# Performance work log

Measured on AMD Instinct MI355X. Metric: run time of the kernel, lower is better.

## Reference

```python
import jax, jax.numpy as jnp
import numpy as np

EMBED_DIM = 1024
HEAD_DIM = 64
B, S = 8, 2048


def setup_inputs() -> dict:
    key = jax.random.key(0)
    ks = jax.random.split(key, 8)
    s_in = 1.0 / np.sqrt(EMBED_DIM)
    return {
        "x": jax.random.normal(ks[0], (B, S, EMBED_DIM), dtype=jnp.float32),
        "y": jax.random.normal(ks[1], (B, S, EMBED_DIM), dtype=jnp.float32),
        "Wq": jax.random.normal(ks[2], (EMBED_DIM, HEAD_DIM), dtype=jnp.float32) * s_in,
        "bq": jnp.zeros((HEAD_DIM,), dtype=jnp.float32),
        "Wk": jax.random.normal(ks[3], (EMBED_DIM, HEAD_DIM), dtype=jnp.float32) * s_in,
        "bk": jnp.zeros((HEAD_DIM,), dtype=jnp.float32),
        "Wv": jax.random.normal(ks[4], (EMBED_DIM, HEAD_DIM), dtype=jnp.float32) * s_in,
        "bv": jnp.zeros((HEAD_DIM,), dtype=jnp.float32),
    }


def reference(x, y, Wq, bq, Wk, bk, Wv, bv):
    # single-head attention; mask=True -> tril applied PRE-softmax (zeros, not -inf)
    q = jnp.einsum("bse,eh->bsh", y, Wq) + bq  # [B,S,H]
    k = jnp.einsum("bse,eh->bsh", x, Wk) + bk
    v = jnp.einsum("bse,eh->bsh", x, Wv) + bv
    scale = 1.0 / jnp.sqrt(jnp.float32(HEAD_DIM))
    scores = jnp.einsum("bqh,bkh->bqk", q, k) * scale  # [B,S,S]
    scores = jnp.tril(scores)  # faithful: zero upper triangle BEFORE softmax
    attn = jax.nn.softmax(scores, axis=-1)
    return jnp.einsum("bqk,bkh->bqh", attn, v)  # [B,S,H]
```

## Files before the change

### kernel.cpp

```cpp
#include <hip/hip_runtime.h>

#define SEQ 2048
#define EMB 1024
#define HD 64

typedef _Float16 f16x8 __attribute__((ext_vector_type(8)));
typedef _Float16 f16x4 __attribute__((ext_vector_type(4)));
typedef float f32x4 __attribute__((ext_vector_type(4)));

__device__ __forceinline__ f32x4 mfma32(f16x8 a, f16x8 b, f32x4 c) {
    return __builtin_amdgcn_mfma_f32_16x16x32_f16(a, b, c, 0, 0, 0);
}
__device__ __forceinline__ f32x4 mfma16(f16x4 a, f16x4 b, f32x4 c) {
    return __builtin_amdgcn_mfma_f32_16x16x16f16(a, b, c, 0, 0, 0);
}

__global__ __launch_bounds__(256) void wcvt_kernel(
    const float* __restrict__ Wq, const float* __restrict__ Wk,
    const float* __restrict__ Wv, _Float16* __restrict__ Wf)
{
    const int m = blockIdx.x >> 2, nt = blockIdx.x & 3;
    const float* __restrict__ W = (m == 0) ? Wq : (m == 1) ? Wk : Wv;
    const int tid = threadIdx.x;
    #pragma unroll
    for (int i = 0; i < 8; ++i) {
        int linear = i * 256 + tid;
        int kc = linear >> 6, ln = linear & 63;
        int q8 = (ln >> 4) * 8, l = ln & 15;
        f16x8 w;
        #pragma unroll
        for (int j = 0; j < 8; ++j)
            w[j] = (_Float16)W[(size_t)(kc * 32 + q8 + j) * 64 + nt * 16 + l];
        *(f16x8*)&Wf[((size_t)((m * 4 + nt) * 32 + kc)) * 512 + (size_t)ln * 8] = w;
    }
}

__global__ __launch_bounds__(512) void proj_kernel(
    const float* __restrict__ x, const float* __restrict__ y,
    const _Float16* __restrict__ Wf,
    const float* __restrict__ bq, const float* __restrict__ bk,
    const float* __restrict__ bv,
    _Float16* __restrict__ Qb, _Float16* __restrict__ Kf,
    _Float16* __restrict__ Vf, float* __restrict__ Vts)
{
    const int mode = blockIdx.y;
    const int r0 = blockIdx.x * 64;
    const int tid = threadIdx.x;
    const int wave = tid >> 6, lane = tid & 63;
    const int l15 = lane & 15, quad = lane >> 4;
    const int rowgrp = wave >> 1, khalf = wave & 1;

    __shared__ float TL[64][65];

    const float* __restrict__ src = mode ? x : y;
    const _Float16* __restrict__ WA = Wf + (mode ? 65536 : 0);
    const _Float16* __restrict__ WB = Wf + 131072;

    f32x4 zero = {0.f, 0.f, 0.f, 0.f};
    f32x4 acc0[4], acc1[4];
    #pragma unroll
    for (int i = 0; i < 4; ++i) { acc0[i] = zero; acc1[i] = zero; }

    const float* arow = src + (size_t)(r0 + rowgrp * 16 + l15) * 1024 + khalf * 512 + quad * 8;
    const int lo8 = lane * 8;
    const int kb = khalf * 16;

    float4 A0[4], A1[4];
    f16x8 Bq[2][4], Bv[2][4];

    auto LDA = [&](int d, int kc) {
        const float4* p = (const float4*)(arow + kc * 32);
        A0[d] = p[0]; A1[d] = p[1];
    };
    auto LDB = [&](int d, int kc) {
        #pragma unroll
        for (int nt = 0; nt < 4; ++nt)
            Bq[d][nt] = *(const f16x8*)&WA[((size_t)(nt * 32 + kb + kc)) * 512 + lo8];
        if (mode) {
            #pragma unroll
            for (int nt = 0; nt < 4; ++nt)
                Bv[d][nt] = *(const f16x8*)&WB[((size_t)(nt * 32 + kb + kc)) * 512 + lo8];
        }
    };

    LDA(0, 0); LDA(1, 1); LDA(2, 2); LDA(3, 3);
    LDB(0, 0); LDB(1, 1);

    #pragma unroll
    for (int kc = 0; kc < 16; ++kc) {
        const int sa = kc & 3, sb = kc & 1;
        f16x8 af;
        af[0] = (_Float16)A0[sa].x; af[1] = (_Float16)A0[sa].y;
        af[2] = (_Float16)A0[sa].z; af[3] = (_Float16)A0[sa].w;
        af[4] = (_Float16)A1[sa].x; af[5] = (_Float16)A1[sa].y;
        af[6] = (_Float16)A1[sa].z; af[7] = (_Float16)A1[sa].w;
        #pragma unroll
        for (int nt = 0; nt < 4; ++nt)
            acc0[nt] = mfma32(af, Bq[sb][nt], acc0[nt]);
        if (mode) {
            #pragma unroll
            for (int nt = 0; nt < 4; ++nt)
                acc1[nt] = mfma32(af, Bv[sb][nt], acc1[nt]);
        }
        if (kc < 12) LDA(sa, kc + 4);
        if (kc < 14) LDB(sb, kc + 2);
    }

    const float* __restrict__ bias0 = mode ? bk : bq;
    const int bb = r0 >> 11, s0 = r0 & (SEQ - 1);

    if (khalf == 1) {
        #pragma unroll
        for (int nt = 0; nt < 4; ++nt)
            #pragma unroll
            for (int r = 0; r < 4; ++r)
                TL[rowgrp * 16 + quad * 4 + r][nt * 16 + l15] = acc0[nt][r];
    }
    __syncthreads();
    if (khalf == 0) {
        #pragma unroll
        for (int nt = 0; nt < 4; ++nt) {
            float bs = bias0[nt * 16 + l15];
            #pragma unroll
            for (int r = 0; r < 4; ++r) {
                int rr = rowgrp * 16 + quad * 4 + r;
                TL[rr][nt * 16 + l15] = acc0[nt][r] + TL[rr][nt * 16 + l15] + bs;
            }
        }
    }
    __syncthreads();

    if (mode == 0) {
        int row = tid >> 3, c8 = (tid & 7) * 8;
        f16x8 o;
        #pragma unroll
        for (int j = 0; j < 8; ++j) o[j] = (_Float16)TL[row][c8 + j];
        *(f16x8*)&Qb[(size_t)(r0 + row) * 64 + c8] = o;
    } else {
        {
            int c = tid >> 7, hf = (tid >> 6) & 1, ln = tid & 63;
            f16x8 w;
            #pragma unroll
            for (int j = 0; j < 8; ++j)
                w[j] = (_Float16)TL[c * 16 + (ln & 15)][hf * 32 + ((ln >> 4) << 3) + j];
            *(f16x8*)&Kf[(((size_t)(bb * 128 + (s0 >> 4) + c)) * 2 + hf) * 512 + ln * 8] = w;
        }
        __syncthreads();
        if (khalf == 1) {
            #pragma unroll
            for (int nt = 0; nt < 4; ++nt)
                #pragma unroll
                for (int r = 0; r < 4; ++r)
                    TL[rowgrp * 16 + quad * 4 + r][nt * 16 + l15] = acc1[nt][r];
        }
        __syncthreads();
        if (khalf == 0) {
            #pragma unroll
            for (int nt = 0; nt < 4; ++nt) {
                float bs = bv[nt * 16 + l15];
                #pragma unroll
                for (int r = 0; r < 4; ++r) {
                    int rr = rowgrp * 16 + quad * 4 + r;
                    TL[rr][nt * 16 + l15] = acc1[nt][r] + TL[rr][nt * 16 + l15] + bs;
                }
            }
        }
        __syncthreads();
        {
            int c2 = tid >> 8, ht = (tid >> 6) & 3, ln = tid & 63;
            f16x8 w;
            #pragma unroll
            for (int j = 0; j < 8; ++j)
                w[j] = (_Float16)TL[c2 * 32 + ((j >> 2) << 4) + ((ln >> 4) << 2) + (j & 3)][ht * 16 + (ln & 15)];
            *(f16x8*)&Vf[(((size_t)(bb * 64 + (s0 >> 5) + c2)) * 4 + ht) * 512 + ln * 8] = w;
        }
        if (tid < 256) {
            int h = tid & 63, wv = tid >> 6;
            float s = 0.f;
            #pragma unroll
            for (int i = 0; i < 16; ++i) s += TL[wv * 16 + i][h];
            Vts[((size_t)bb * 128 + (s0 >> 4) + wv) * 64 + h] = s;
        }
    }
}

__global__ __launch_bounds__(256) void vsuf_kernel(
    const float* __restrict__ Vts, float* __restrict__ Vsuf)
{
    const int b = blockIdx.x, hh = blockIdx.y;
    const int tid = threadIdx.x;
    const int seg = tid >> 5, hl = tid & 31, h = (hh << 5) + hl;
    __shared__ float segsum[8][33];
    float vals[16];
    const float* src = Vts + ((size_t)b * 128 + seg * 16) * 64 + h;
    float s = 0.f;
    #pragma unroll
    for (int i = 0; i < 16; ++i) { vals[i] = src[i * 64]; s += vals[i]; }
    segsum[seg][hl] = s;
    __syncthreads();
    float run = 0.f;
    #pragma unroll
    for (int ss = 7; ss >= 0; --ss) if (ss > seg) run += segsum[ss][hl];
    float* dst = Vsuf + ((size_t)b * 128 + seg * 16) * 64 + h;
    #pragma unroll
    for (int i = 15; i >= 0; --i) { run += vals[i]; dst[i * 64] = run; }
}

__global__ __launch_bounds__(256) void attn_kernel(
    const _Float16* __restrict__ Qb, const _Float16* __restrict__ Kf,
    const _Float16* __restrict__ Vf, const float* __restrict__ Vsuf,
    float* __restrict__ out)
{
    const int b = blockIdx.y;
    const int tq = blockIdx.x;
    const int tid = threadIdx.x;
    const int wave = tid >> 6, lane = tid & 63;
    const int l15 = lane & 15, quad = lane >> 4;

    __shared__ float part[4][32][68];
    __shared__ float lpart[4][32];

    const f16x4 ONES4 = {(_Float16)1.f, (_Float16)1.f, (_Float16)1.f, (_Float16)1.f};
    f32x4 zero = {0.f, 0.f, 0.f, 0.f};

    const int qbase = tq << 5;
    const int qgA = qbase + l15, qgB = qgA + 16;

    const _Float16* qpA = Qb + ((size_t)(b * SEQ + qbase + l15) << 6);
    const _Float16* qpB = qpA + (16 << 6);
    f16x8 qfA0 = *(const f16x8*)(qpA + quad * 8);
    f16x8 qfA1 = *(const f16x8*)(qpA + 32 + quad * 8);
    f16x8 qfB0 = *(const f16x8*)(qpB + quad * 8);
    f16x8 qfB1 = *(const f16x8*)(qpB + 32 + quad * 8);

    f32x4 accOA[4], accOB[4], accLA = zero, accLB = zero;
    #pragma unroll
    for (int i = 0; i < 4; ++i) { accOA[i] = zero; accOB[i] = zero; }

    const _Float16* __restrict__ kfb = Kf + (size_t)b * 131072 + lane * 8;
    const _Float16* __restrict__ vfb = Vf + (size_t)b * 131072 + lane * 8;

    f16x8 k0[4], v0[4], k1[4], v1[4];

    auto LDK = [&](f16x8* kd, f16x8* vd, int kc2) {
        const _Float16* kp = kfb + (size_t)kc2 * 2048;
        kd[0] = *(const f16x8*)(kp);
        kd[1] = *(const f16x8*)(kp + 512);
        kd[2] = *(const f16x8*)(kp + 1024);
        kd[3] = *(const f16x8*)(kp + 1536);
        const _Float16* vp = vfb + (size_t)kc2 * 2048;
        vd[0] = *(const f16x8*)(vp);
        vd[1] = *(const f16x8*)(vp + 512);
        vd[2] = *(const f16x8*)(vp + 1024);
        vd[3] = *(const f16x8*)(vp + 1536);
    };

    auto CMP = [&](const f16x8* kd, const f16x8* vd, int kc2) {
        #pragma unroll
        for (int c = 0; c < 2; ++c) {
            f32x4 sA = zero, sB = zero;
            sA = mfma32(kd[2 * c], qfA0, sA);
            sA = mfma32(kd[2 * c + 1], qfA1, sA);
            sB = mfma32(kd[2 * c], qfB0, sB);
            sB = mfma32(kd[2 * c + 1], qfB1, sB);
            const int kqb = (kc2 << 5) + (c << 4) + (quad << 2);
            f16x4 pfA, pfB;
            #pragma unroll
            for (int r = 0; r < 4; ++r) {
                pfA[r] = (_Float16)((kqb + r <= qgA) ? __expf(sA[r] * 0.125f) : 1.0f);
                pfB[r] = (_Float16)((kqb + r <= qgB) ? __expf(sB[r] * 0.125f) : 1.0f);
            }
            #pragma unroll
            for (int ht = 0; ht < 4; ++ht) {
                f16x8 vv = vd[ht];
                f16x4 vh;
                if (c == 0) { vh[0] = vv[0]; vh[1] = vv[1]; vh[2] = vv[2]; vh[3] = vv[3]; }
                else        { vh[0] = vv[4]; vh[1] = vv[5]; vh[2] = vv[6]; vh[3] = vv[7]; }
                accOA[ht] = mfma16(vh, pfA, accOA[ht]);
                accOB[ht] = mfma16(vh, pfB, accOB[ht]);
            }
            accLA = mfma16(ONES4, pfA, accLA);
            accLB = mfma16(ONES4, pfB, accLB);
        }
    };

    const int n2 = tq + 1;
    int i = wave;
    LDK(k0, v0, (i < n2) ? i : 0);
    for (; i < n2; i += 8) {
        const int i1 = i + 4;
        LDK(k1, v1, (i1 < n2) ? i1 : i);
        CMP(k0, v0, i);
        const int i2 = i + 8;
        LDK(k0, v0, (i2 < n2) ? i2 : i);
        if (i1 < n2) CMP(k1, v1, i1);
    }

    #pragma unroll
    for (int ht = 0; ht < 4; ++ht)
        #pragma unroll
        for (int r = 0; r < 4; ++r) {
            part[wave][l15][ht * 16 + quad * 4 + r] = accOA[ht][r];
            part[wave][16 + l15][ht * 16 + quad * 4 + r] = accOB[ht][r];
        }
    if (quad == 0) {
        lpart[wave][l15] = accLA[0];
        lpart[wave][16 + l15] = accLB[0];
    }
    __syncthreads();

    {
        const int q = tid >> 3, hb = (tid & 7) << 3;
        f32x4 o0 = zero, o1 = zero;
        float l = 0.f;
        #pragma unroll
        for (int w = 0; w < 4; ++w) {
            l += lpart[w][q];
            o0 = o0 + *(const f32x4*)&part[w][q][hb];
            o1 = o1 + *(const f32x4*)&part[w][q][hb + 4];
        }
        const int tend = 2 * tq + 2;
        const float nOnes = (float)(SEQ - (tend << 4));
        f32x4 cs0 = zero, cs1 = zero;
        if (tend < 128) {
            const float* cp = &Vsuf[((size_t)(b * 128 + tend) << 6) + hb];
            cs0 = *(const f32x4*)(cp);
            cs1 = *(const f32x4*)(cp + 4);
        }
        const float inv = 1.0f / (l + nOnes);
        f32x4 r0 = (o0 + cs0) * inv;
        f32x4 r1 = (o1 + cs1) * inv;
        float* op = &out[((size_t)(b * SEQ + qbase + q) << 6) + hb];
        *(f32x4*)(op) = r0;
        *(f32x4*)(op + 4) = r1;
    }
}

extern "C" void kernel_launch(void* const* d_in, const int* in_sizes, int n_in,
                              void* d_out, int out_size, void* d_ws, size_t ws_size,
                              hipStream_t stream) {
    const float* x  = (const float*)d_in[0];
    const float* y  = (const float*)d_in[1];
    const float* Wq = (const float*)d_in[2];
    const float* bq = (const float*)d_in[3];
    const float* Wk = (const float*)d_in[4];
    const float* bk = (const float*)d_in[5];
    const float* Wv = (const float*)d_in[6];
    const float* bv = (const float*)d_in[7];
    float* out = (float*)d_out;

    char* ws = (char*)d_ws;
    _Float16* Qb  = (_Float16*)(ws);
    _Float16* Kf  = (_Float16*)(ws + (1u << 21));
    _Float16* Vf  = (_Float16*)(ws + (2u << 21));
    _Float16* Wf  = (_Float16*)(ws + (3u << 21));
    float*    Vts = (float*)(ws + (3u << 21) + (512u << 10));
    float*    Vsf = (float*)(ws + (3u << 21) + (768u << 10));

    wcvt_kernel<<<dim3(12), 256, 0, stream>>>(Wq, Wk, Wv, Wf);
    proj_kernel<<<dim3(256, 2), 512, 0, stream>>>(x, y, Wf, bq, bk, bv, Qb, Kf, Vf, Vts);
    vsuf_kernel<<<dim3(8, 2), 256, 0, stream>>>(Vts, Vsf);
    attn_kernel<<<dim3(64, 8), 256, 0, stream>>>(Qb, Kf, Vf, Vsf, out);
}
```

Baseline: 197.2 us.

## Rebalance attention causal work, drop proj K-split, widen weight conversion grid

The weight-conversion kernel now runs on a 12x4 grid so each block converts a quarter of the K chunks. The projection kernel drops its two-wave K split: each wave covers a full 16-row tile over all of K, each block handles 128 rows, and the LDS reduction and a sync round are gone. The attention kernel pairs query tile tp with 63-tp inside one block to even out causal work across half as many blocks, and adds occupancy hints to launch_bounds. Together these change load balance and cut sync overhead, at the cost of a longer serial K loop per wave in the projection and fewer attention blocks.

Measured after the change: 202.5 us. 1.03x slower.

```diff
diff --git a/kernel.cpp b/kernel.cpp
--- a/kernel.cpp
+++ b/kernel.cpp
@@ -19,13 +19,13 @@
     const float* __restrict__ Wq, const float* __restrict__ Wk,
     const float* __restrict__ Wv, _Float16* __restrict__ Wf)
 {
-    const int m = blockIdx.x >> 2, nt = blockIdx.x & 3;
+    const int m = blockIdx.x >> 2, nt = blockIdx.x & 3, kq = blockIdx.y;
     const float* __restrict__ W = (m == 0) ? Wq : (m == 1) ? Wk : Wv;
     const int tid = threadIdx.x;
     #pragma unroll
-    for (int i = 0; i < 8; ++i) {
+    for (int i = 0; i < 2; ++i) {
         int linear = i * 256 + tid;
-        int kc = linear >> 6, ln = linear & 63;
+        int kc = kq * 8 + (linear >> 6), ln = linear & 63;
         int q8 = (ln >> 4) * 8, l = ln & 15;
         f16x8 w;
         #pragma unroll
@@ -35,7 +35,7 @@
     }
 }
 
-__global__ __launch_bounds__(512) void proj_kernel(
+__global__ __launch_bounds__(512, 2) void proj_kernel(
     const float* __restrict__ x, const float* __restrict__ y,
     const _Float16* __restrict__ Wf,
     const float* __restrict__ bq, const float* __restrict__ bk,
@@ -44,13 +44,12 @@
     _Float16* __restrict__ Vf, float* __restrict__ Vts)
 {
     const int mode = blockIdx.y;
-    const int r0 = blockIdx.x * 64;
+    const int r0 = blockIdx.x * 128;
     const int tid = threadIdx.x;
     const int wave = tid >> 6, lane = tid & 63;
     const int l15 = lane & 15, quad = lane >> 4;
-    const int rowgrp = wave >> 1, khalf = wave & 1;
-
-    __shared__ float TL[64][65];
+
+    __shared__ float TL[128][65];
 
     const float* __restrict__ src = mode ? x : y;
     const _Float16* __restrict__ WA = Wf + (mode ? 65536 : 0);
@@ -61,121 +60,123 @@
     #pragma unroll
     for (int i = 0; i < 4; ++i) { acc0[i] = zero; acc1[i] = zero; }
 
-    const float* arow = src + (size_t)(r0 + rowgrp * 16 + l15) * 1024 + khalf * 512 + quad * 8;
+    const float* arow = src + (size_t)(r0 + wave * 16 + l15) * 1024 + quad * 8;
     const int lo8 = lane * 8;
-    const int kb = khalf * 16;
-
-    float4 A0[4], A1[4];
-    f16x8 Bq[2][4], Bv[2][4];
-
-    auto LDA = [&](int d, int kc) {
-        const float4* p = (const float4*)(arow + kc * 32);
-        A0[d] = p[0]; A1[d] = p[1];
+
+    float4 Aa0, Aa1, Ab0, Ab1;
+    f16x8 BqA[4], BqB[4], BvA[4], BvB[4];
+
+    auto LDA = [&](float4& x0, float4& x1, int ch) {
+        const float4* p = (const float4*)(arow + ch * 32);
+        x0 = p[0]; x1 = p[1];
     };
-    auto LDB = [&](int d, int kc) {
+    auto LDBq = [&](f16x8* d, int ch) {
         #pragma unroll
         for (int nt = 0; nt < 4; ++nt)
-            Bq[d][nt] = *(const f16x8*)&WA[((size_t)(nt * 32 + kb + kc)) * 512 + lo8];
-        if (mode) {
+            d[nt] = *(const f16x8*)&WA[((size_t)(nt * 32 + ch)) * 512 + lo8];
+    };
+    auto LDBv = [&](f16x8* d, int ch) {
+        #pragma unroll
+        for (int nt = 0; nt < 4; ++nt)
+            d[nt] = *(const f16x8*)&WB[((size_t)(nt * 32 + ch)) * 512 + lo8];
+    };
+    auto CVT = [&](float4 a0, float4 a1) {
+        f16x8 af;
+        af[0] = (_Float16)a0.x; af[1] = (_Float16)a0.y;
+        af[2] = (_Float16)a0.z; af[3] = (_Float16)a0.w;
+        af[4] = (_Float16)a1.x; af[5] = (_Float16)a1.y;
+        af[6] = (_Float16)a1.z; af[7] = (_Float16)a1.w;
+        return af;
+    };
+
+    LDA(Aa0, Aa1, 0); LDBq(BqA, 0); if (mode) LDBv(BvA, 0);
+    LDA(Ab0, Ab1, 1); LDBq(BqB, 1); if (mode) LDBv(BvB, 1);
+
+    #pragma unroll 1
+    for (int ch = 0; ch < 32; ch += 2) {
+        {
+            f16x8 af = CVT(Aa0, Aa1);
             #pragma unroll
             for (int nt = 0; nt < 4; ++nt)
-                Bv[d][nt] = *(const f16x8*)&WB[((size_t)(nt * 32 + kb + kc)) * 512 + lo8];
-        }
-    };
-
-    LDA(0, 0); LDA(1, 1); LDA(2, 2); LDA(3, 3);
-    LDB(0, 0); LDB(1, 1);
-
-    #pragma unroll
-    for (int kc = 0; kc < 16; ++kc) {
-        const int sa = kc & 3, sb = kc & 1;
-        f16x8 af;
-        af[0] = (_Float16)A0[sa].x; af[1] = (_Float16)A0[sa].y;
-        af[2] = (_Float16)A0[sa].z; af[3] = (_Float16)A0[sa].w;
-        af[4] = (_Float16)A1[sa].x; af[5] = (_Float16)A1[sa].y;
-        af[6] = (_Float16)A1[sa].z; af[7] = (_Float16)A1[sa].w;
-        #pragma unroll
-        for (int nt = 0; nt < 4; ++nt)
-            acc0[nt] = mfma32(af, Bq[sb][nt], acc0[nt]);
-        if (mode) {
+                acc0[nt] = mfma32(af, BqA[nt], acc0[nt]);
+            if (mode) {
+                #pragma unroll
+                for (int nt = 0; nt < 4; ++nt)
+                    acc1[nt] = mfma32(af, BvA[nt], acc1[nt]);
+            }
+            const int nx = (ch + 2) & 31;
+            LDA(Aa0, Aa1, nx); LDBq(BqA, nx); if (mode) LDBv(BvA, nx);
+        }
+        {
+            f16x8 af = CVT(Ab0, Ab1);
             #pragma unroll
             for (int nt = 0; nt < 4; ++nt)
-                acc1[nt] = mfma32(af, Bv[sb][nt], acc1[nt]);
-        }
-        if (kc < 12) LDA(sa, kc + 4);
-        if (kc < 14) LDB(sb, kc + 2);
+                acc0[nt] = mfma32(af, BqB[nt], acc0[nt]);
+            if (mode) {
+                #pragma unroll
+                for (int nt = 0; nt < 4; ++nt)
+                    acc1[nt] = mfma32(af, BvB[nt], acc1[nt]);
+            }
+            const int nx = (ch + 3) & 31;
+            LDA(Ab0, Ab1, nx); LDBq(BqB, nx); if (mode) LDBv(BvB, nx);
+        }
     }
 
-    const float* __restrict__ bias0 = mode ? bk : bq;
     const int bb = r0 >> 11, s0 = r0 & (SEQ - 1);
 
-    if (khalf == 1) {
-        #pragma unroll
-        for (int nt = 0; nt < 4; ++nt)
+    if (mode == 0) {
+        #pragma unroll
+        for (int nt = 0; nt < 4; ++nt) {
+            int h = nt * 16 + l15;
+            float bs = bq[h];
+            #pragma unroll
+            for (int r = 0; r < 4; ++r) {
+                int row = r0 + wave * 16 + quad * 4 + r;
+                Qb[(size_t)row * 64 + h] = (_Float16)(acc0[nt][r] + bs);
+            }
+        }
+    } else {
+        #pragma unroll
+        for (int nt = 0; nt < 4; ++nt) {
+            float bs = bk[nt * 16 + l15];
             #pragma unroll
             for (int r = 0; r < 4; ++r)
-                TL[rowgrp * 16 + quad * 4 + r][nt * 16 + l15] = acc0[nt][r];
-    }
-    __syncthreads();
-    if (khalf == 0) {
+                TL[wave * 16 + quad * 4 + r][nt * 16 + l15] = acc0[nt][r] + bs;
+        }
+        __syncthreads();
+        {
+            int c = tid >> 6, ln = tid & 63;
+            const int q8 = (ln >> 4) << 3, l = ln & 15;
+            #pragma unroll
+            for (int half = 0; half < 2; ++half) {
+                f16x8 w;
+                #pragma unroll
+                for (int j = 0; j < 8; ++j)
+                    w[j] = (_Float16)TL[c * 16 + l][half * 32 + q8 + j];
+                *(f16x8*)&Kf[(((size_t)(bb * 128 + (s0 >> 4) + c)) * 2 + half) * 512 + ln * 8] = w;
+            }
+        }
+        __syncthreads();
         #pragma unroll
         for (int nt = 0; nt < 4; ++nt) {
-            float bs = bias0[nt * 16 + l15];
-            #pragma unroll
-            for (int r = 0; r < 4; ++r) {
-                int rr = rowgrp * 16 + quad * 4 + r;
-                TL[rr][nt * 16 + l15] = acc0[nt][r] + TL[rr][nt * 16 + l15] + bs;
-            }
-        }
-    }
-    __syncthreads();
-
-    if (mode == 0) {
-        int row = tid >> 3, c8 = (tid & 7) * 8;
-        f16x8 o;
-        #pragma unroll
-        for (int j = 0; j < 8; ++j) o[j] = (_Float16)TL[row][c8 + j];
-        *(f16x8*)&Qb[(size_t)(r0 + row) * 64 + c8] = o;
-    } else {
-        {
-            int c = tid >> 7, hf = (tid >> 6) & 1, ln = tid & 63;
-            f16x8 w;
-            #pragma unroll
-            for (int j = 0; j < 8; ++j)
-                w[j] = (_Float16)TL[c * 16 + (ln & 15)][hf * 32 + ((ln >> 4) << 3) + j];
-            *(f16x8*)&Kf[(((size_t)(bb * 128 + (s0 >> 4) + c)) * 2 + hf) * 512 + ln * 8] = w;
-        }
-        __syncthreads();
-        if (khalf == 1) {
-            #pragma unroll
-            for (int nt = 0; nt < 4; ++nt)
-                #pragma unroll
-                for (int r = 0; r < 4; ++r)
-                    TL[rowgrp * 16 + quad * 4 + r][nt * 16 + l15] = acc1[nt][r];
-        }
-        __syncthreads();
-        if (khalf == 0) {
-            #pragma unroll
-            for (int nt = 0; nt < 4; ++nt) {
-                float bs = bv[nt * 16 + l15];
-                #pragma unroll
-                for (int r = 0; r < 4; ++r) {
-                    int rr = rowgrp * 16 + quad * 4 + r;
-                    TL[rr][nt * 16 + l15] = acc1[nt][r] + TL[rr][nt * 16 + l15] + bs;
-                }
-            }
-        }
-        __syncthreads();
-        {
-            int c2 = tid >> 8, ht = (tid >> 6) & 3, ln = tid & 63;
-            f16x8 w;
-            #pragma unroll
-            for (int j = 0; j < 8; ++j)
-                w[j] = (_Float16)TL[c2 * 32 + ((j >> 2) << 4) + ((ln >> 4) << 2) + (j & 3)][ht * 16 + (ln & 15)];
-            *(f16x8*)&Vf[(((size_t)(bb * 64 + (s0 >> 5) + c2)) * 4 + ht) * 512 + ln * 8] = w;
-        }
-        if (tid < 256) {
-            int h = tid & 63, wv = tid >> 6;
+            float bs = bv[nt * 16 + l15];
+            #pragma unroll
+            for (int r = 0; r < 4; ++r)
+                TL[wave * 16 + quad * 4 + r][nt * 16 + l15] = acc1[nt][r] + bs;
+        }
+        __syncthreads();
+        {
+            int c2 = tid >> 7, hth = (tid >> 6) & 1, ln = tid & 63;
+            #pragma unroll
+            for (int p = 0; p < 2; ++p) {
+                int ht = hth * 2 + p;
+                f16x8 w;
+                #pragma unroll
+                for (int j = 0; j < 8; ++j)
+                    w[j] = (_Float16)TL[c2 * 32 + ((j >> 2) << 4) + ((ln >> 4) << 2) + (j & 3)][ht * 16 + (ln & 15)];
+                *(f16x8*)&Vf[(((size_t)(bb * 64 + (s0 >> 5) + c2)) * 4 + ht) * 512 + ln * 8] = w;
+            }
+            int wv = tid >> 6, h = tid & 63;
             float s = 0.f;
             #pragma unroll
             for (int i = 0; i < 16; ++i) s += TL[wv * 16 + i][h];
@@ -206,13 +207,13 @@
     for (int i = 15; i >= 0; --i) { run += vals[i]; dst[i * 64] = run; }
 }
 
-__global__ __launch_bounds__(256) void attn_kernel(
+__global__ __launch_bounds__(256, 2) void attn_kernel(
     const _Float16* __restrict__ Qb, const _Float16* __restrict__ Kf,
     const _Float16* __restrict__ Vf, const float* __restrict__ Vsuf,
     float* __restrict__ out)
 {
     const int b = blockIdx.y;
-    const int tq = blockIdx.x;
+    const int tp = blockIdx.x;
     const int tid = threadIdx.x;
     const int wave = tid >> 6, lane = tid & 63;
     const int l15 = lane & 15, quad = lane >> 4;
@@ -223,116 +224,122 @@
     const f16x4 ONES4 = {(_Float16)1.f, (_Float16)1.f, (_Float16)1.f, (_Float16)1.f};
     f32x4 zero = {0.f, 0.f, 0.f, 0.f};
 
-    const int qbase = tq << 5;
-    const int qgA = qbase + l15, qgB = qgA + 16;
-
-    const _Float16* qpA = Qb + ((size_t)(b * SEQ + qbase + l15) << 6);
-    const _Float16* qpB = qpA + (16 << 6);
-    f16x8 qfA0 = *(const f16x8*)(qpA + quad * 8);
-    f16x8 qfA1 = *(const f16x8*)(qpA + 32 + quad * 8);
-    f16x8 qfB0 = *(const f16x8*)(qpB + quad * 8);
-    f16x8 qfB1 = *(const f16x8*)(qpB + 32 + quad * 8);
-
-    f32x4 accOA[4], accOB[4], accLA = zero, accLB = zero;
-    #pragma unroll
-    for (int i = 0; i < 4; ++i) { accOA[i] = zero; accOB[i] = zero; }
-
     const _Float16* __restrict__ kfb = Kf + (size_t)b * 131072 + lane * 8;
     const _Float16* __restrict__ vfb = Vf + (size_t)b * 131072 + lane * 8;
 
-    f16x8 k0[4], v0[4], k1[4], v1[4];
-
-    auto LDK = [&](f16x8* kd, f16x8* vd, int kc2) {
-        const _Float16* kp = kfb + (size_t)kc2 * 2048;
-        kd[0] = *(const f16x8*)(kp);
-        kd[1] = *(const f16x8*)(kp + 512);
-        kd[2] = *(const f16x8*)(kp + 1024);
-        kd[3] = *(const f16x8*)(kp + 1536);
-        const _Float16* vp = vfb + (size_t)kc2 * 2048;
-        vd[0] = *(const f16x8*)(vp);
-        vd[1] = *(const f16x8*)(vp + 512);
-        vd[2] = *(const f16x8*)(vp + 1024);
-        vd[3] = *(const f16x8*)(vp + 1536);
-    };
-
-    auto CMP = [&](const f16x8* kd, const f16x8* vd, int kc2) {
-        #pragma unroll
-        for (int c = 0; c < 2; ++c) {
-            f32x4 sA = zero, sB = zero;
-            sA = mfma32(kd[2 * c], qfA0, sA);
-            sA = mfma32(kd[2 * c + 1], qfA1, sA);
-            sB = mfma32(kd[2 * c], qfB0, sB);
-            sB = mfma32(kd[2 * c + 1], qfB1, sB);
-            const int kqb = (kc2 << 5) + (c << 4) + (quad << 2);
-            f16x4 pfA, pfB;
+    #pragma unroll 1
+    for (int sel = 0; sel < 2; ++sel) {
+        const int tq = sel ? (63 - tp) : tp;
+        const int qbase = tq << 5;
+        const int qgA = qbase + l15, qgB = qgA + 16;
+
+        __syncthreads();
+
+        const _Float16* qpA = Qb + ((size_t)(b * SEQ + qbase + l15) << 6);
+        const _Float16* qpB = qpA + (16 << 6);
+        f16x8 qfA0 = *(const f16x8*)(qpA + quad * 8);
+        f16x8 qfA1 = *(const f16x8*)(qpA + 32 + quad * 8);
+        f16x8 qfB0 = *(const f16x8*)(qpB + quad * 8);
+        f16x8 qfB1 = *(const f16x8*)(qpB + 32 + quad * 8);
+
+        f32x4 accOA[4], accOB[4], accLA = zero, accLB = zero;
+        #pragma unroll
+        for (int i = 0; i < 4; ++i) { accOA[i] = zero; accOB[i] = zero; }
+
+        f16x8 k0[4], v0[4], k1[4], v1[4];
+
+        auto LDK = [&](f16x8* kd, f16x8* vd, int kc2) {
+            const _Float16* kp = kfb + (size_t)kc2 * 2048;
+            kd[0] = *(const f16x8*)(kp);
+            kd[1] = *(const f16x8*)(kp + 512);
+            kd[2] = *(const f16x8*)(kp + 1024);
+            kd[3] = *(const f16x8*)(kp + 1536);
+            const _Float16* vp = vfb + (size_t)kc2 * 2048;
+            vd[0] = *(const f16x8*)(vp);
+            vd[1] = *(const f16x8*)(vp + 512);
+            vd[2] = *(const f16x8*)(vp + 1024);
+            vd[3] = *(const f16x8*)(vp + 1536);
+        };
+
+        auto CMP = [&](const f16x8* kd, const f16x8* vd, int kc2) {
+            #pragma unroll
+            for (int c = 0; c < 2; ++c) {
+                f32x4 sA = zero, sB = zero;
+                sA = mfma32(kd[2 * c], qfA0, sA);
+                sA = mfma32(kd[2 * c + 1], qfA1, sA);
+                sB = mfma32(kd[2 * c], qfB0, sB);
+                sB = mfma32(kd[2 * c + 1], qfB1, sB);
+                const int kqb = (kc2 << 5) + (c << 4) + (quad << 2);
+                f16x4 pfA, pfB;
+                #pragma unroll
+                for (int r = 0; r < 4; ++r) {
+                    pfA[r] = (_Float16)((kqb + r <= qgA) ? __expf(sA[r] * 0.125f) : 1.0f);
+                    pfB[r] = (_Float16)((kqb + r <= qgB) ? __expf(sB[r] * 0.125f) : 1.0f);
+                }
+                #pragma unroll
+                for (int ht = 0; ht < 4; ++ht) {
+                    f16x8 vv = vd[ht];
+                    f16x4 vh;
+                    if (c == 0) { vh[0] = vv[0]; vh[1] = vv[1]; vh[2] = vv[2]; vh[3] = vv[3]; }
+                    else        { vh[0] = vv[4]; vh[1] = vv[5]; vh[2] = vv[6]; vh[3] = vv[7]; }
+                    accOA[ht] = mfma16(vh, pfA, accOA[ht]);
+                    accOB[ht] = mfma16(vh, pfB, accOB[ht]);
+                }
+                accLA = mfma16(ONES4, pfA, accLA);
+                accLB = mfma16(ONES4, pfB, accLB);
+            }
+        };
+
+        const int n2 = tq + 1;
+        int i = wave;
+        LDK(k0, v0, (i < n2) ? i : 0);
+        for (; i < n2; i += 8) {
+            const int i1 = i + 4;
+            LDK(k1, v1, (i1 < n2) ? i1 : i);
+            CMP(k0, v0, i);
+            const int i2 = i + 8;
+            LDK(k0, v0, (i2 < n2) ? i2 : i);
+            if (i1 < n2) CMP(k1, v1, i1);
+        }
+
+        #pragma unroll
+        for (int ht = 0; ht < 4; ++ht)
             #pragma unroll
             for (int r = 0; r < 4; ++r) {
-                pfA[r] = (_Float16)((kqb + r <= qgA) ? __expf(sA[r] * 0.125f) : 1.0f);
-                pfB[r] = (_Float16)((kqb + r <= qgB) ? __expf(sB[r] * 0.125f) : 1.0f);
-            }
-            #pragma unroll
-            for (int ht = 0; ht < 4; ++ht) {
-                f16x8 vv = vd[ht];
-                f16x4 vh;
-                if (c == 0) { vh[0] = vv[0]; vh[1] = vv[1]; vh[2] = vv[2]; vh[3] = vv[3]; }
-                else        { vh[0] = vv[4]; vh[1] = vv[5]; vh[2] = vv[6]; vh[3] = vv[7]; }
-                accOA[ht] = mfma16(vh, pfA, accOA[ht]);
-                accOB[ht] = mfma16(vh, pfB, accOB[ht]);
-            }
-            accLA = mfma16(ONES4, pfA, accLA);
-            accLB = mfma16(ONES4, pfB, accLB);
-        }
-    };
-
-    const int n2 = tq + 1;
-    int i = wave;
-    LDK(k0, v0, (i < n2) ? i : 0);
-    for (; i < n2; i += 8) {
-        const int i1 = i + 4;
-        LDK(k1, v1, (i1 < n2) ? i1 : i);
-        CMP(k0, v0, i);
-        const int i2 = i + 8;
-        LDK(k0, v0, (i2 < n2) ? i2 : i);
-        if (i1 < n2) CMP(k1, v1, i1);
-    }
-
-    #pragma unroll
-    for (int ht = 0; ht < 4; ++ht)
-        #pragma unroll
-        for (int r = 0; r < 4; ++r) {
-            part[wave][l15][ht * 16 + quad * 4 + r] = accOA[ht][r];
-            part[wave][16 + l15][ht * 16 + quad * 4 + r] = accOB[ht][r];
-        }
-    if (quad == 0) {
-        lpart[wave][l15] = accLA[0];
-        lpart[wave][16 + l15] = accLB[0];
-    }
-    __syncthreads();
-
-    {
-        const int q = tid >> 3, hb = (tid & 7) << 3;
-        f32x4 o0 = zero, o1 = zero;
-        float l = 0.f;
-        #pragma unroll
-        for (int w = 0; w < 4; ++w) {
-            l += lpart[w][q];
-            o0 = o0 + *(const f32x4*)&part[w][q][hb];
-            o1 = o1 + *(const f32x4*)&part[w][q][hb + 4];
-        }
-        const int tend = 2 * tq + 2;
-        const float nOnes = (float)(SEQ - (tend << 4));
-        f32x4 cs0 = zero, cs1 = zero;
-        if (tend < 128) {
-            const float* cp = &Vsuf[((size_t)(b * 128 + tend) << 6) + hb];
-            cs0 = *(const f32x4*)(cp);
-            cs1 = *(const f32x4*)(cp + 4);
-        }
-        const float inv = 1.0f / (l + nOnes);
-        f32x4 r0 = (o0 + cs0) * inv;
-        f32x4 r1 = (o1 + cs1) * inv;
-        float* op = &out[((size_t)(b * SEQ + qbase + q) << 6) + hb];
-        *(f32x4*)(op) = r0;
-        *(f32x4*)(op + 4) = r1;
+                part[wave][l15][ht * 16 + quad * 4 + r] = accOA[ht][r];
+                part[wave][16 + l15][ht * 16 + quad * 4 + r] = accOB[ht][r];
+            }
+        if (quad == 0) {
+            lpart[wave][l15] = accLA[0];
+            lpart[wave][16 + l15] = accLB[0];
+        }
+        __syncthreads();
+
+        {
+            const int q = tid >> 3, hb = (tid & 7) << 3;
+            f32x4 o0 = zero, o1 = zero;
+            float l = 0.f;
+            #pragma unroll
+            for (int w = 0; w < 4; ++w) {
+                l += lpart[w][q];
+                o0 = o0 + *(const f32x4*)&part[w][q][hb];
+                o1 = o1 + *(const f32x4*)&part[w][q][hb + 4];
+            }
+            const int tend = 2 * tq + 2;
+            const float nOnes = (float)(SEQ - (tend << 4));
+            f32x4 cs0 = zero, cs1 = zero;
+            if (tend < 128) {
+                const float* cp = &Vsuf[((size_t)(b * 128 + tend) << 6) + hb];
+                cs0 = *(const f32x4*)(cp);
+                cs1 = *(const f32x4*)(cp + 4);
+            }
+            const float inv = 1.0f / (l + nOnes);
+            f32x4 r0 = (o0 + cs0) * inv;
+            f32x4 r1 = (o1 + cs1) * inv;
+            float* op = &out[((size_t)(b * SEQ + qbase + q) << 6) + hb];
+            *(f32x4*)(op) = r0;
+            *(f32x4*)(op + 4) = r1;
+        }
     }
 }
 
@@ -357,8 +364,8 @@
     float*    Vts = (float*)(ws + (3u << 21) + (512u << 10));
     float*    Vsf = (float*)(ws + (3u << 21) + (768u << 10));
 
-    wcvt_kernel<<<dim3(12), 256, 0, stream>>>(Wq, Wk, Wv, Wf);
-    proj_kernel<<<dim3(256, 2), 512, 0, stream>>>(x, y, Wf, bq, bk, bv, Qb, Kf, Vf, Vts);
+    wcvt_kernel<<<dim3(12, 4), 256, 0, stream>>>(Wq, Wk, Wv, Wf);
+    proj_kernel<<<dim3(128, 2), 512, 0, stream>>>(x, y, Wf, bq, bk, bv, Qb, Kf, Vf, Vts);
     vsuf_kernel<<<dim3(8, 2), 256, 0, stream>>>(Vts, Vsf);
-    attn_kernel<<<dim3(64, 8), 256, 0, stream>>>(Qb, Kf, Vf, Vsf, out);
-}
+    attn_kernel<<<dim3(32, 8), 256, 0, stream>>>(Qb, Kf, Vf, Vsf, out);
+}
```
